# Optimization experiments

Measured on AMD Instinct MI355X. Metric: run time of the kernel, lower is better.

The kernel has to match this reference:

```python
import jax, jax.numpy as jnp
import numpy as np

DIM = 512
NHEADS = 8
HEAD_DIM = DIM // NHEADS
LN_EPS = 1e-5


def _layernorm(x, g, b):
    m = jnp.mean(x, axis=-1, keepdims=True)
    v = jnp.mean((x - m) ** 2, axis=-1, keepdims=True)
    return (x - m) * jax.lax.rsqrt(v + LN_EPS) * g + b


def setup_inputs() -> dict:
    key = jax.random.key(0)
    ks = jax.random.split(key, 12)
    s = 1.0 / np.sqrt(DIM)
    inp = {
        "x": jax.random.normal(ks[0], (4, 2048, DIM), dtype=jnp.float32),
        "Wq": jax.random.uniform(ks[1], (DIM, DIM), jnp.float32, -s, s),
        "bq": jnp.zeros((DIM,), jnp.float32),
        "Wk": jax.random.uniform(ks[2], (DIM, DIM), jnp.float32, -s, s),
        "bk": jnp.zeros((DIM,), jnp.float32),
        "Wv": jax.random.uniform(ks[3], (DIM, DIM), jnp.float32, -s, s),
        "bv": jnp.zeros((DIM,), jnp.float32),
        "Wo": jax.random.uniform(ks[4], (DIM, DIM), jnp.float32, -s, s),
        "bo": jnp.zeros((DIM,), jnp.float32),
        "W1": jax.random.uniform(ks[5], (DIM, 2 * DIM), jnp.float32, -s, s),
        "b1": jnp.zeros((2 * DIM,), jnp.float32),
        "W2": jax.random.uniform(ks[6], (2 * DIM, DIM), jnp.float32, -1.0 / np.sqrt(2 * DIM), 1.0 / np.sqrt(2 * DIM)),
        "b2": jnp.zeros((DIM,), jnp.float32),
        "g1": jnp.ones((DIM,), jnp.float32),
        "be1": jnp.zeros((DIM,), jnp.float32),
        "g2": jnp.ones((DIM,), jnp.float32),
        "be2": jnp.zeros((DIM,), jnp.float32),
    }
    return inp


def reference(x, Wq, bq, Wk, bk, Wv, bv, Wo, bo, W1, b1, W2, b2, g1, be1, g2, be2):
    # norm_before=True path; dropout disabled (inference)
    bsz, n, _ = x.shape
    res = x
    xn = _layernorm(x, g1, be1)

    def proj(W, b):
        return (xn @ W + b).reshape(bsz, n, NHEADS, HEAD_DIM).transpose(0, 2, 1, 3)  # (B,H,N,D)

    q = proj(Wq, bq) / np.sqrt(HEAD_DIM).astype(np.float32)
    k = proj(Wk, bk)
    v = proj(Wv, bv)

    q = jax.nn.elu(q) + 1.0
    k = jax.nn.elu(k) + 1.0

    # quadratic score as in the original module (B,H,N,N)
    score = jnp.einsum("bhnd,bhmd->bhnm", q, k)
    denom = jnp.sum(score, axis=-1, keepdims=True) + 1e-5
    score = score / denom
    out = jnp.einsum("bhnm,bhmd->bhnd", score, v)

    out = out.transpose(0, 2, 1, 3).reshape(bsz, n, DIM)
    out = out @ Wo + bo
    out = res + out

    res2 = out
    h = _layernorm(out, g2, be2)
    h = jax.nn.relu(h @ W1 + b1) @ W2 + b2
    return res2 + h
```

## Files before the change

kernel.cpp:

```cpp
#include <hip/hip_runtime.h>
#include <hip/hip_bf16.h>
#include <math.h>

#define DIM 512
#define HEADS 8
#define HD 64
#define ROWS_TOTAL 8192
#define SEQ 2048
#define NSLICE 16

typedef __hip_bfloat16 bf16;
typedef __bf16 bf16x8 __attribute__((ext_vector_type(8)));
typedef float f32x4 __attribute__((ext_vector_type(4)));

__device__ __forceinline__ float elu1(float x) {
    return x > 0.f ? x + 1.f : __expf(x);
}
__device__ __forceinline__ void gl16(const void* g, void* l) {
    __builtin_amdgcn_global_load_lds(
        (const __attribute__((address_space(1))) void*)g,
        (__attribute__((address_space(3))) void*)l, 16, 0, 0);
}
__device__ __forceinline__ unsigned short f2bu(float v) {
    bf16 t = __float2bfloat16(v);
    return *(unsigned short*)&t;
}

__global__ __launch_bounds__(256) void prep_kernel(
    const float* __restrict__ Wq, const float* __restrict__ Wk,
    const float* __restrict__ Wv, const float* __restrict__ Wo,
    const float* __restrict__ W1, const float* __restrict__ W2,
    bf16* WqkvT, bf16* WoT, bf16* W1T, bf16* W2T,
    const float* __restrict__ x, const float* __restrict__ g,
    const float* __restrict__ b, bf16* __restrict__ xout,
    bf16* __restrict__ xb)
{
    __shared__ float t[32][33];
    int bx = blockIdx.x;
    if (bx >= 2048) {
        int row  = (bx - 2048) * 4 + (threadIdx.x >> 6);
        int lane = threadIdx.x & 63;
        const float* xr = x + (size_t)row * DIM + lane * 8;
        float4 v1 = *(const float4*)xr;
        float4 v2 = *(const float4*)(xr + 4);
        float f[8] = {v1.x, v1.y, v1.z, v1.w, v2.x, v2.y, v2.z, v2.w};
        int c = lane * 8;
        bf16 rb[8];
#pragma unroll
        for (int j = 0; j < 8; ++j) rb[j] = __float2bfloat16(f[j]);
        *(uint4*)(xb + (size_t)row * DIM + c) = *(uint4*)rb;
        float s = 0.f, sq = 0.f;
#pragma unroll
        for (int j = 0; j < 8; ++j) { s += f[j]; sq += f[j]*f[j]; }
#pragma unroll
        for (int off = 32; off > 0; off >>= 1) {
            s  += __shfl_xor(s,  off, 64);
            sq += __shfl_xor(sq, off, 64);
        }
        float mean = s * (1.f / DIM);
        float var  = sq * (1.f / DIM) - mean * mean;
        float rstd = rsqrtf(var + 1e-5f);
        float4 ga = *(const float4*)(g + c);
        float4 gb = *(const float4*)(g + c + 4);
        float4 ba = *(const float4*)(b + c);
        float4 bb = *(const float4*)(b + c + 4);
        float gg[8]  = {ga.x,ga.y,ga.z,ga.w,gb.x,gb.y,gb.z,gb.w};
        float bbv[8] = {ba.x,ba.y,ba.z,ba.w,bb.x,bb.y,bb.z,bb.w};
        bf16 ob[8];
#pragma unroll
        for (int j = 0; j < 8; ++j)
            ob[j] = __float2bfloat16((f[j] - mean) * rstd * gg[j] + bbv[j]);
        *(uint4*)(xout + (size_t)row * DIM + c) = *(uint4*)ob;
        return;
    }
    const float* W; bf16* T; int K, N, tk, tn, mode = 0;
    if (bx < 1024) {
        int m = bx >> 8, tix = bx & 255;
        const float* ws_[4] = {Wq, Wk, Wv, Wo};
        W = ws_[m];
        T = (m == 3) ? WoT : WqkvT;
        mode = (m == 1) ? 1 : (m == 2 ? 2 : 0);
        K = 512; N = 512; tn = tix & 15; tk = tix >> 4;
    } else if (bx < 1536) {
        int tix = bx - 1024; W = W1; T = W1T; K = 512; N = 1024; tn = tix & 31; tk = tix >> 5;
    } else {
        int tix = bx - 1536; W = W2; T = W2T; K = 1024; N = 512; tn = tix & 15; tk = tix >> 4;
    }
    int n0 = tn * 32, k0 = tk * 32;
    int tx = threadIdx.x & 31, ty = threadIdx.x >> 5;
#pragma unroll
    for (int i = 0; i < 32; i += 8)
        t[ty + i][tx] = W[(size_t)(k0 + ty + i) * N + n0 + tx];
    __syncthreads();
#pragma unroll
    for (int i = 0; i < 32; i += 8) {
        int n = n0 + ty + i;
        int dr = n;
        if (mode == 1)      dr = 512 + ((n >> 6) << 7) + (n & 63);
        else if (mode == 2) dr = 576 + ((n >> 6) << 7) + (n & 63);
        T[(size_t)dr * K + k0 + tx] = __float2bfloat16(t[tx][ty + i]);
    }
}

__global__ __launch_bounds__(256) void ln_kernel(const bf16* __restrict__ xv,
                                                 const float* __restrict__ g,
                                                 const float* __restrict__ b,
                                                 bf16* __restrict__ out)
{
    int row  = blockIdx.x * 4 + (threadIdx.x >> 6);
    int lane = threadIdx.x & 63;
    bf16x8 v = *(const bf16x8*)(xv + (size_t)row * DIM + lane * 8);
    float f[8];
#pragma unroll
    for (int j = 0; j < 8; ++j) f[j] = (float)v[j];
    float s = 0.f, sq = 0.f;
#pragma unroll
    for (int j = 0; j < 8; ++j) { s += f[j]; sq += f[j]*f[j]; }
#pragma unroll
    for (int off = 32; off > 0; off >>= 1) {
        s  += __shfl_xor(s,  off, 64);
        sq += __shfl_xor(sq, off, 64);
    }
    float mean = s * (1.f / DIM);
    float var  = sq * (1.f / DIM) - mean * mean;
    float rstd = rsqrtf(var + 1e-5f);
    int c = lane * 8;
    float4 ga = *(const float4*)(g + c);
    float4 gb = *(const float4*)(g + c + 4);
    float4 ba = *(const float4*)(b + c);
    float4 bb = *(const float4*)(b + c + 4);
    float gg[8]  = {ga.x,ga.y,ga.z,ga.w,gb.x,gb.y,gb.z,gb.w};
    float bbv[8] = {ba.x,ba.y,ba.z,ba.w,bb.x,bb.y,bb.z,bb.w};
    bf16 ob[8];
#pragma unroll
    for (int j = 0; j < 8; ++j)
        ob[j] = __float2bfloat16((f[j] - mean) * rstd * gg[j] + bbv[j]);
    *(uint4*)(out + (size_t)row * DIM + c) = *(uint4*)ob;
}

__global__ __launch_bounds__(256) void qkv_kv_kernel(
    const bf16* __restrict__ A, const bf16* __restrict__ Bt,
    const float* __restrict__ bq, const float* __restrict__ bk,
    const float* __restrict__ bv, bf16* __restrict__ Qb,
    float* __restrict__ KVTp, float* __restrict__ KSp, float scale)
{
    constexpr int K = 512;
    __shared__ __align__(16) bf16 As[2][128 * 64];
    __shared__ __align__(16) bf16 Bs[2][128 * 64];
    int tid = threadIdx.x;
    int lane = tid & 63, wid = tid >> 6;
    int wr = wid >> 1, wc = wid & 1;
    int cpx = gridDim.x >> 3;
    int work = (blockIdx.x & 7) * cpx + (blockIdx.x >> 3);
    int bx = work % 12, by = work / 12;
    int m0 = by * 128, n0 = bx * 128;
    int sr = tid >> 3;
    int scb = (((tid & 7) << 4) ^ ((sr & 7) << 4)) >> 1;
    const bf16* ga = A  + (size_t)(m0 + sr) * K + scb;
    const bf16* gb = Bt + (size_t)(n0 + sr) * K + scb;
    f32x4 acc[4][4] = {};
    int la = lane & 15, ka = lane >> 4;
    int xo = (la & 7) << 4;

#pragma unroll
    for (int j = 0; j < 4; ++j) {
        gl16(ga + (size_t)j * 32 * K, &As[0][tid * 8 + j * 2048]);
        gl16(gb + (size_t)j * 32 * K, &Bs[0][tid * 8 + j * 2048]);
    }
    __syncthreads();
    for (int t = 0; t < 8; ++t) {
        int cur = t & 1;
        if (t + 1 < 8) {
            int k0 = (t + 1) << 6;
#pragma unroll
            for (int j = 0; j < 4; ++j) {
                gl16(ga + (size_t)j * 32 * K + k0, &As[cur ^ 1][tid * 8 + j * 2048]);
                gl16(gb + (size_t)j * 32 * K + k0, &Bs[cur ^ 1][tid * 8 + j * 2048]);
            }
        }
        const char* Ab = (const char*)As[cur];
        const char* Bb = (const char*)Bs[cur];
        bf16x8 a[2][4], b[2][4];
#pragma unroll
        for (int kk = 0; kk < 2; ++kk) {
            int kb = (kk * 64 + ka * 16) ^ xo;
#pragma unroll
            for (int m = 0; m < 4; ++m)
                a[kk][m] = *(const bf16x8*)(Ab + (wr * 64 + m * 16 + la) * 128 + kb);
#pragma unroll
            for (int n = 0; n < 4; ++n)
                b[kk][n] = *(const bf16x8*)(Bb + (wc * 64 + n * 16 + la) * 128 + kb);
        }
#pragma unroll
        for (int kk = 0; kk < 2; ++kk)
#pragma unroll
            for (int m = 0; m < 4; ++m)
#pragma unroll
                for (int n = 0; n < 4; ++n)
                    acc[m][n] = __builtin_amdgcn_mfma_f32_16x16x32_bf16(a[kk][m], b[kk][n], acc[m][n], 0, 0, 0);
        __syncthreads();
    }

    int rg = (lane >> 4) * 4;
    if (bx < 4) {
#pragma unroll
        for (int m = 0; m < 4; ++m) {
            int gm = m0 + wr * 64 + m * 16 + rg;
#pragma unroll
            for (int n = 0; n < 4; ++n) {
                int gnl = bx * 128 + wc * 64 + n * 16 + la;
                float bv_ = bq[gnl];
#pragma unroll
                for (int j = 0; j < 4; ++j) {
                    float v = elu1((acc[m][n][j] + bv_) * scale);
                    Qb[(size_t)(gm + j) * 512 + gnl] = __float2bfloat16(v);
                }
            }
        }
    } else {
        int hh = bx - 4;
        int bb = m0 >> 11, sl = (m0 >> 7) & 15;
        int bh = bb * 8 + hh;
        bf16* KT = (bf16*)As;
        bf16* VT = KT + 8192;
        const float* bias = (wc == 0) ? (bk + hh * 64) : (bv + hh * 64);
        bf16* base = (wc == 0) ? KT : VT;
#pragma unroll
        for (int m = 0; m < 4; ++m) {
            int r0 = wr * 64 + m * 16 + rg;
#pragma unroll
            for (int n = 0; n < 4; ++n) {
                int col = n * 16 + la;
                float bv_ = bias[col];
                ushort4 pk;
                unsigned short* pp = (unsigned short*)&pk;
#pragma unroll
                for (int j = 0; j < 4; ++j) {
                    float v = acc[m][n][j] + bv_;
                    if (wc == 0) v = elu1(v);
                    pp[j] = f2bu(v);
                }
                int byteoff = col * 256 + ((r0 * 2) ^ ((col & 7) << 4));
                *(ushort4*)((char*)base + byteoff) = pk;
            }
        }
        __syncthreads();
        f32x4 acc2[4] = {};
        int fe = wid;
#pragma unroll
        for (int kk = 0; kk < 4; ++kk) {
            int kbyte = kk * 64 + ka * 16;
            int ar = fe * 16 + la;
            bf16x8 av = *(const bf16x8*)((char*)VT + ar * 256 + (kbyte ^ ((ar & 7) << 4)));
#pragma unroll
            for (int fd = 0; fd < 4; ++fd) {
                int br = fd * 16 + la;
                bf16x8 bk8 = *(const bf16x8*)((char*)KT + br * 256 + (kbyte ^ ((br & 7) << 4)));
                acc2[fd] = __builtin_amdgcn_mfma_f32_16x16x32_bf16(av, bk8, acc2[fd], 0, 0, 0);
            }
        }
        float* dst = KVTp + (size_t)(bh * 16 + sl) * 4096;
#pragma unroll
        for (int fd = 0; fd < 4; ++fd)
#pragma unroll
            for (int j = 0; j < 4; ++j)
                dst[(fe * 16 + rg + j) * 64 + fd * 16 + la] = acc2[fd][j];
        if (tid < 64) {
            float s = 0.f;
#pragma unroll
            for (int rc = 0; rc < 16; ++rc) {
                bf16x8 kv8 = *(const bf16x8*)((char*)KT + tid * 256 + ((rc * 16) ^ ((tid & 7) << 4)));
#pragma unroll
                for (int j = 0; j < 8; ++j) s += (float)kv8[j];
            }
            KSp[(size_t)(bh * 16 + sl) * 64 + tid] = s;
        }
    }
}

template<int BM, int BN, int EPI>
__global__ __launch_bounds__(256) void mfma_gemm(
    const bf16* __restrict__ A, const bf16* __restrict__ Bt,
    const float* __restrict__ b0, const bf16* __restrict__ resid,
    void* __restrict__ O0, int N, int K, int GX)
{
    constexpr int MW = BM / 32;
    constexpr int NW = BN / 32;
    __shared__ __align__(16) bf16 As[2][BM * 64];
    __shared__ __align__(16) bf16 Bs[2][BN * 64];
    int tid = threadIdx.x;
    int lane = tid & 63, wid = tid >> 6;
    int wr = wid >> 1, wc = wid & 1;
    int cpx = gridDim.x >> 3;
    int work = (blockIdx.x & 7) * cpx + (blockIdx.x >> 3);
    int bx = work % GX, by = work / GX;
    int m0 = by * BM, n0 = bx * BN;
    int sr = tid >> 3;
    int scb = (((tid & 7) << 4) ^ ((sr & 7) << 4)) >> 1;
    const bf16* ga = A  + (size_t)(m0 + sr) * K + scb;
    const bf16* gb = Bt + (size_t)(n0 + sr) * K + scb;
    f32x4 acc[MW][NW] = {};
    int la = lane & 15, ka = lane >> 4;
    int xo = (la & 7) << 4;
    int nt = K >> 6;

#pragma unroll
    for (int j = 0; j < MW; ++j)
        gl16(ga + (size_t)j * 32 * K, &As[0][tid * 8 + j * 2048]);
#pragma unroll
    for (int j = 0; j < NW; ++j)
        gl16(gb + (size_t)j * 32 * K, &Bs[0][tid * 8 + j * 2048]);
    __syncthreads();

    for (int t = 0; t < nt; ++t) {
        int cur = t & 1;
        if (t + 1 < nt) {
            int k0 = (t + 1) << 6;
#pragma unroll
            for (int j = 0; j < MW; ++j)
                gl16(ga + (size_t)j * 32 * K + k0, &As[cur ^ 1][tid * 8 + j * 2048]);
#pragma unroll
            for (int j = 0; j < NW; ++j)
                gl16(gb + (size_t)j * 32 * K + k0, &Bs[cur ^ 1][tid * 8 + j * 2048]);
        }
        const char* Ab = (const char*)As[cur];
        const char* Bb = (const char*)Bs[cur];
        bf16x8 a[2][MW], b[2][NW];
#pragma unroll
        for (int kk = 0; kk < 2; ++kk) {
            int kb = (kk * 64 + ka * 16) ^ xo;
#pragma unroll
            for (int m = 0; m < MW; ++m)
                a[kk][m] = *(const bf16x8*)(Ab + (wr * (BM/2) + m * 16 + la) * 128 + kb);
#pragma unroll
            for (int n = 0; n < NW; ++n)
                b[kk][n] = *(const bf16x8*)(Bb + (wc * (BN/2) + n * 16 + la) * 128 + kb);
        }
#pragma unroll
        for (int kk = 0; kk < 2; ++kk)
#pragma unroll
            for (int m = 0; m < MW; ++m)
#pragma unroll
                for (int n = 0; n < NW; ++n)
                    acc[m][n] = __builtin_amdgcn_mfma_f32_16x16x32_bf16(a[kk][m], b[kk][n], acc[m][n], 0, 0, 0);
        __syncthreads();
    }

    int rg = (lane >> 4) * 4;
#pragma unroll
    for (int m = 0; m < MW; ++m) {
        int gm = m0 + wr * (BM/2) + m * 16 + rg;
#pragma unroll
        for (int n = 0; n < NW; ++n) {
            int gn = n0 + wc * (BN/2) + n * 16 + la;
            float bv_ = b0[gn];
#pragma unroll
            for (int j = 0; j < 4; ++j) {
                float v = acc[m][n][j] + bv_;
                if (EPI == 3) v = fmaxf(v, 0.f);
                if ((EPI == 0 || EPI == 2) && resid)
                    v += (float)resid[(size_t)(gm + j) * N + gn];
                if (EPI == 0) ((float*)O0)[(size_t)(gm + j) * N + gn] = v;
                else          ((bf16*)O0)[(size_t)(gm + j) * N + gn] = __float2bfloat16(v);
            }
        }
    }
}

__global__ __launch_bounds__(256) void attn_gemm(
    const bf16* __restrict__ Q, const float* __restrict__ KVTp,
    const float* __restrict__ KSp, bf16* __restrict__ out)
{
    __shared__ __align__(16) bf16 As[128][72];
    __shared__ __align__(16) bf16 Bs[64][72];
    __shared__ float ks[64];
    __shared__ float dn[128];
    int h = blockIdx.x;
    int m0 = blockIdx.y * 128;
    int bh = ((m0 >> 11) << 3) + h;
    int tid = threadIdx.x;
    int lane = tid & 63, wid = tid >> 6;
    {
        int r = tid >> 3, c0 = (tid & 7) * 8;
#pragma unroll
        for (int p = 0; p < 4; ++p) {
            int row = p * 32 + r;
            *(bf16x8*)&As[row][c0] =
                *(const bf16x8*)(Q + (size_t)(m0 + row) * DIM + h * HD + c0);
        }
        const float* kvb = KVTp + (size_t)bh * 16 * 4096;
        int e = tid & 63, d0 = (tid >> 6) * 16;
        float s_[16] = {};
#pragma unroll
        for (int sl = 0; sl < NSLICE; ++sl) {
            const float* p = kvb + sl * 4096 + e * 64 + d0;
#pragma unroll
            for (int i = 0; i < 16; ++i) s_[i] += p[i];
        }
#pragma unroll
        for (int i = 0; i < 16; ++i)
            Bs[e][d0 + i] = __float2bfloat16(s_[i]);
        if (tid < 64) {
            float s = 0.f;
#pragma unroll
            for (int sl = 0; sl < NSLICE; ++sl)
                s += KSp[(size_t)(bh * 16 + sl) * 64 + tid];
            ks[tid] = s;
        }
    }
    __syncthreads();
    if (tid < 128) {
        float s = 0.f;
#pragma unroll
        for (int c = 0; c < 8; ++c) {
            bf16x8 qv = *(const bf16x8*)&As[tid][c * 8];
#pragma unroll
            for (int j = 0; j < 8; ++j)
                s += (float)qv[j] * ks[c * 8 + j];
        }
        dn[tid] = 1.f / (s + 1e-5f);
    }
    int la = lane & 15, ka = lane >> 4;
    f32x4 acc[2][4] = {};
#pragma unroll
    for (int s = 0; s < 2; ++s) {
        bf16x8 a[2], b[4];
#pragma unroll
        for (int m = 0; m < 2; ++m)
            a[m] = *(const bf16x8*)&As[wid * 32 + m * 16 + la][s * 32 + ka * 8];
#pragma unroll
        for (int n = 0; n < 4; ++n)
            b[n] = *(const bf16x8*)&Bs[n * 16 + la][s * 32 + ka * 8];
#pragma unroll
        for (int m = 0; m < 2; ++m)
#pragma unroll
            for (int n = 0; n < 4; ++n)
                acc[m][n] = __builtin_amdgcn_mfma_f32_16x16x32_bf16(a[m], b[n], acc[m][n], 0, 0, 0);
    }
    __syncthreads();
    int rg = (lane >> 4) * 4;
#pragma unroll
    for (int m = 0; m < 2; ++m) {
#pragma unroll
        for (int j = 0; j < 4; ++j) {
            int lr = wid * 32 + m * 16 + rg + j;
            float rdn = dn[lr];
            int gm = m0 + lr;
#pragma unroll
            for (int n = 0; n < 4; ++n) {
                int gn = h * HD + n * 16 + la;
                out[(size_t)gm * DIM + gn] = __float2bfloat16(acc[m][n][j] * rdn);
            }
        }
    }
}

extern "C" void kernel_launch(void* const* d_in, const int* in_sizes, int n_in,
                              void* d_out, int out_size, void* d_ws, size_t ws_size,
                              hipStream_t stream)
{
    const float* x   = (const float*)d_in[0];
    const float* Wq  = (const float*)d_in[1];
    const float* bq  = (const float*)d_in[2];
    const float* Wk  = (const float*)d_in[3];
    const float* bk  = (const float*)d_in[4];
    const float* Wv  = (const float*)d_in[5];
    const float* bv  = (const float*)d_in[6];
    const float* Wo  = (const float*)d_in[7];
    const float* bo  = (const float*)d_in[8];
    const float* W1  = (const float*)d_in[9];
    const float* b1  = (const float*)d_in[10];
    const float* W2  = (const float*)d_in[11];
    const float* b2  = (const float*)d_in[12];
    const float* g1  = (const float*)d_in[13];
    const float* be1 = (const float*)d_in[14];
    const float* g2  = (const float*)d_in[15];
    const float* be2 = (const float*)d_in[16];

    char* wsb = (char*)d_ws;
    const size_t MB = 1u << 20;
    bf16*  Qb  = (bf16*)(wsb + 0 * MB);
    bf16*  xn  = (bf16*)(wsb + 8 * MB);
    bf16*  yb  = (bf16*)(wsb + 16 * MB);
    bf16*  hb  = (bf16*)(wsb + 24 * MB);
    bf16*  WqkvT = (bf16*)(wsb + 32 * MB);
    bf16*  WoT = WqkvT + 1536 * 512;
    bf16*  W1T = WoT + 512 * 512;
    bf16*  W2T = W1T + 1024 * 512;
    float* KVTp = (float*)(wsb + 40 * MB);
    float* KSp  = (float*)(wsb + 48 * MB);
    bf16*  xb   = (bf16*)(wsb + 49 * MB);
    bf16*  F1  = (bf16*)(wsb + 0 * MB);
    bf16*  attnb = xn;

    float* out = (float*)d_out;
    dim3 blk(256);

    prep_kernel<<<4096, blk, 0, stream>>>(Wq, Wk, Wv, Wo, W1, W2,
                                          WqkvT, WoT, W1T, W2T, x, g1, be1, xn, xb);
    qkv_kv_kernel<<<768, blk, 0, stream>>>(xn, WqkvT, bq, bk, bv,
                                           Qb, KVTp, KSp, 0.125f);
    attn_gemm<<<dim3(8, 64), blk, 0, stream>>>(Qb, KVTp, KSp, attnb);
    mfma_gemm<64, 64, 2><<<1024, blk, 0, stream>>>(
        attnb, WoT, bo, xb, yb, 512, 512, 8);
    ln_kernel<<<2048, blk, 0, stream>>>(yb, g2, be2, hb);
    mfma_gemm<64, 64, 3><<<2048, blk, 0, stream>>>(
        hb, W1T, b1, nullptr, F1, 1024, 512, 16);
    mfma_gemm<64, 64, 0><<<1024, blk, 0, stream>>>(
        F1, W2T, b2, yb, out, 512, 1024, 8);
}
```

Measured before the change: 120.6 us.

## Triple-buffer GEMM K-loop with vmcnt waits and read fp32 residual directly

The MFMA GEMM moves from double to triple LDS buffering, prefetching two K-tiles ahead. It swaps __syncthreads for explicit s_waitcnt vmcnt counts plus s_barrier so more global-to-LDS loads can be in flight. Separately, prep_kernel no longer writes a bf16 copy of x; the Wo GEMM epilogue reads the fp32 input x as the residual instead. This drops a write pass and improves residual precision, but the residual read doubles in bytes and LDS use per block grows by half, which may lower occupancy.

```diff
diff --git a/kernel.cpp b/kernel.cpp
--- a/kernel.cpp
+++ b/kernel.cpp
@@ -32,8 +32,7 @@
     const float* __restrict__ W1, const float* __restrict__ W2,
     bf16* WqkvT, bf16* WoT, bf16* W1T, bf16* W2T,
     const float* __restrict__ x, const float* __restrict__ g,
-    const float* __restrict__ b, bf16* __restrict__ xout,
-    bf16* __restrict__ xb)
+    const float* __restrict__ b, bf16* __restrict__ xout)
 {
     __shared__ float t[32][33];
     int bx = blockIdx.x;
@@ -45,10 +44,6 @@
         float4 v2 = *(const float4*)(xr + 4);
         float f[8] = {v1.x, v1.y, v1.z, v1.w, v2.x, v2.y, v2.z, v2.w};
         int c = lane * 8;
-        bf16 rb[8];
-#pragma unroll
-        for (int j = 0; j < 8; ++j) rb[j] = __float2bfloat16(f[j]);
-        *(uint4*)(xb + (size_t)row * DIM + c) = *(uint4*)rb;
         float s = 0.f, sq = 0.f;
 #pragma unroll
         for (int j = 0; j < 8; ++j) { s += f[j]; sq += f[j]*f[j]; }
@@ -281,13 +276,15 @@
 template<int BM, int BN, int EPI>
 __global__ __launch_bounds__(256) void mfma_gemm(
     const bf16* __restrict__ A, const bf16* __restrict__ Bt,
-    const float* __restrict__ b0, const bf16* __restrict__ resid,
-    void* __restrict__ O0, int N, int K, int GX)
+    const float* __restrict__ b0, const float* __restrict__ residf,
+    const bf16* __restrict__ residb, void* __restrict__ O0,
+    int N, int K, int GX)
 {
     constexpr int MW = BM / 32;
     constexpr int NW = BN / 32;
-    __shared__ __align__(16) bf16 As[2][BM * 64];
-    __shared__ __align__(16) bf16 Bs[2][BN * 64];
+    constexpr int NL = MW + NW;
+    __shared__ __align__(16) bf16 As[3][BM * 64];
+    __shared__ __align__(16) bf16 Bs[3][BN * 64];
     int tid = threadIdx.x;
     int lane = tid & 63, wid = tid >> 6;
     int wr = wid >> 1, wc = wid & 1;
@@ -304,24 +301,28 @@
     int xo = (la & 7) << 4;
     int nt = K >> 6;
 
-#pragma unroll
-    for (int j = 0; j < MW; ++j)
-        gl16(ga + (size_t)j * 32 * K, &As[0][tid * 8 + j * 2048]);
-#pragma unroll
-    for (int j = 0; j < NW; ++j)
-        gl16(gb + (size_t)j * 32 * K, &Bs[0][tid * 8 + j * 2048]);
-    __syncthreads();
-
+    auto stage = [&](int s, int k0) {
+#pragma unroll
+        for (int j = 0; j < MW; ++j)
+            gl16(ga + (size_t)j * 32 * K + k0, &As[s][tid * 8 + j * 2048]);
+#pragma unroll
+        for (int j = 0; j < NW; ++j)
+            gl16(gb + (size_t)j * 32 * K + k0, &Bs[s][tid * 8 + j * 2048]);
+    };
+
+    stage(0, 0);
+    stage(1, 64);
+
+    int cur = 0;
     for (int t = 0; t < nt; ++t) {
-        int cur = t & 1;
-        if (t + 1 < nt) {
-            int k0 = (t + 1) << 6;
-#pragma unroll
-            for (int j = 0; j < MW; ++j)
-                gl16(ga + (size_t)j * 32 * K + k0, &As[cur ^ 1][tid * 8 + j * 2048]);
-#pragma unroll
-            for (int j = 0; j < NW; ++j)
-                gl16(gb + (size_t)j * 32 * K + k0, &Bs[cur ^ 1][tid * 8 + j * 2048]);
+        if (t + 2 < nt) {
+            int nx = cur + 2; if (nx >= 3) nx -= 3;
+            stage(nx, (t + 2) << 6);
+            asm volatile("s_waitcnt vmcnt(%0)\ns_barrier" :: "n"(2 * NL) : "memory");
+        } else if (t + 1 < nt) {
+            asm volatile("s_waitcnt vmcnt(%0)\ns_barrier" :: "n"(NL) : "memory");
+        } else {
+            asm volatile("s_waitcnt vmcnt(0)\ns_barrier" ::: "memory");
         }
         const char* Ab = (const char*)As[cur];
         const char* Bb = (const char*)Bs[cur];
@@ -343,7 +344,8 @@
 #pragma unroll
                 for (int n = 0; n < NW; ++n)
                     acc[m][n] = __builtin_amdgcn_mfma_f32_16x16x32_bf16(a[kk][m], b[kk][n], acc[m][n], 0, 0, 0);
-        __syncthreads();
+        asm volatile("s_barrier" ::: "memory");
+        ++cur; if (cur >= 3) cur = 0;
     }
 
     int rg = (lane >> 4) * 4;
@@ -358,8 +360,10 @@
             for (int j = 0; j < 4; ++j) {
                 float v = acc[m][n][j] + bv_;
                 if (EPI == 3) v = fmaxf(v, 0.f);
-                if ((EPI == 0 || EPI == 2) && resid)
-                    v += (float)resid[(size_t)(gm + j) * N + gn];
+                if (EPI == 0 && residb)
+                    v += (float)residb[(size_t)(gm + j) * N + gn];
+                if (EPI == 2 && residf)
+                    v += residf[(size_t)(gm + j) * N + gn];
                 if (EPI == 0) ((float*)O0)[(size_t)(gm + j) * N + gn] = v;
                 else          ((bf16*)O0)[(size_t)(gm + j) * N + gn] = __float2bfloat16(v);
             }
@@ -489,7 +493,6 @@
     bf16*  W2T = W1T + 1024 * 512;
     float* KVTp = (float*)(wsb + 40 * MB);
     float* KSp  = (float*)(wsb + 48 * MB);
-    bf16*  xb   = (bf16*)(wsb + 49 * MB);
     bf16*  F1  = (bf16*)(wsb + 0 * MB);
     bf16*  attnb = xn;
 
@@ -497,15 +500,15 @@
     dim3 blk(256);
 
     prep_kernel<<<4096, blk, 0, stream>>>(Wq, Wk, Wv, Wo, W1, W2,
-                                          WqkvT, WoT, W1T, W2T, x, g1, be1, xn, xb);
+                                          WqkvT, WoT, W1T, W2T, x, g1, be1, xn);
     qkv_kv_kernel<<<768, blk, 0, stream>>>(xn, WqkvT, bq, bk, bv,
                                            Qb, KVTp, KSp, 0.125f);
     attn_gemm<<<dim3(8, 64), blk, 0, stream>>>(Qb, KVTp, KSp, attnb);
     mfma_gemm<64, 64, 2><<<1024, blk, 0, stream>>>(
-        attnb, WoT, bo, xb, yb, 512, 512, 8);
+        attnb, WoT, bo, x, nullptr, yb, 512, 512, 8);
     ln_kernel<<<2048, blk, 0, stream>>>(yb, g2, be2, hb);
     mfma_gemm<64, 64, 3><<<2048, blk, 0, stream>>>(
-        hb, W1T, b1, nullptr, F1, 1024, 512, 16);
+        hb, W1T, b1, nullptr, nullptr, F1, 1024, 512, 16);
     mfma_gemm<64, 64, 0><<<1024, blk, 0, stream>>>(
-        F1, W2T, b2, yb, out, 512, 1024, 8);
-}
+        F1, W2T, b2, nullptr, yb, out, 512, 1024, 8);
+}
```

Result: slower. 138.3 us (+14.7%).
